# Optimization experiments

Hardware: AMD Instinct MI355X
Metric: run time of the kernel (lower is better)

## Reference

```python
import jax, jax.numpy as jnp
import numpy as np

NODE_IN, EDGE_IN, OUT, EHID, NSTEPS = 74, 13, 64, 128, 6
LN_EPS = 1e-5


def layer_norm(x, gamma, beta):
    mu = jnp.mean(x, axis=-1, keepdims=True)
    var = jnp.mean((x - mu) ** 2, axis=-1, keepdims=True)
    return (x - mu) * jax.lax.rsqrt(var + LN_EPS) * gamma + beta


def setup_inputs() -> dict:
    key = jax.random.key(0)
    ks = jax.random.split(key, 16)
    V, E = 50000, 100000
    inp = {
        "node_feats": jax.random.normal(ks[0], (V, NODE_IN), jnp.float32),
        "edge_feats": jax.random.normal(ks[1], (E, EDGE_IN), jnp.float32),
        "src": jax.random.randint(ks[2], (E,), 0, V, jnp.int32),
        "dst": jax.random.randint(ks[3], (E,), 0, V, jnp.int32),
        # project_node_feats Linear
        "Wp": jax.random.normal(ks[4], (NODE_IN, OUT), jnp.float32) * 0.1,
        "bp": jnp.zeros((OUT,), jnp.float32),
        # edge network MLP: edge_in -> edge_hidden -> out*out
        "We1": jax.random.normal(ks[5], (EDGE_IN, EHID), jnp.float32) * 0.1,
        "be1": jnp.zeros((EHID,), jnp.float32),
        "We2": jax.random.normal(ks[6], (EHID, OUT * OUT), jnp.float32) * 0.02,
        "be2": jnp.zeros((OUT * OUT,), jnp.float32),
        # NNConv bias
        "bconv": jnp.zeros((OUT,), jnp.float32),
        # linearB: 2*out -> out
        "WB": jax.random.normal(ks[7], (2 * OUT, OUT), jnp.float32) * 0.1,
        "bB": jnp.zeros((OUT,), jnp.float32),
        # LayerNorm
        "gamma": jnp.ones((OUT,), jnp.float32),
        "beta": jnp.zeros((OUT,), jnp.float32),
    }
    return inp


def reference(node_feats, edge_feats, src, dst, Wp, bp, We1, be1, We2, be2,
              bconv, WB, bB, gamma, beta):
    V = node_feats.shape[0]
    # project node feats
    h = jax.nn.relu(node_feats @ Wp + bp)  # (V, OUT)
    # per-edge weight matrices (same every step; edge MLP is step-invariant)
    W_e = (jax.nn.relu(edge_feats @ We1 + be1) @ We2 + be2)
    W_e = W_e.reshape(-1, OUT, OUT)  # (E, OUT, OUT)
    for _ in range(NSTEPS):
        msg = jnp.einsum('ei,eio->eo', h[src], W_e)  # gather + per-edge matmul
        agg = jax.ops.segment_sum(msg, dst, num_segments=V) + bconv
        h = jax.nn.relu(agg)
    atom_feats = h
    pair = jnp.concatenate([h[src], h[dst]], axis=1)  # (E, 2*OUT)
    bond_feats = pair @ WB + bB
    atom_out = layer_norm(atom_feats, gamma, beta)
    bond_out = layer_norm(bond_feats, gamma, beta)
    return (atom_out, bond_out)
```

## Files before the change

kernel.cpp:

```cpp
#include <hip/hip_runtime.h>
#include <hip/hip_bf16.h>

typedef __hip_bfloat16 bf16;
typedef __attribute__((ext_vector_type(8))) short bf16x8;
typedef __attribute__((ext_vector_type(4))) float f32x4;

#define NODE_IN 74
#define EDGE_IN 13
#define OUT     64
#define EHID    128
#define NSTEPS  6
#define LN_EPS  1e-5f
#define MB      128
#define NCHUNK  129
#define CHB     16384

__device__ __forceinline__ float ldv(const bf16* p, size_t i) { return __bfloat162float(p[i]); }
__device__ __forceinline__ float ldv(const float* p, size_t i) { return p[i]; }

__device__ __forceinline__ float waveSum(float v) {
    v += __shfl_xor(v, 32);
    v += __shfl_xor(v, 16);
    v += __shfl_xor(v, 8);
    v += __shfl_xor(v, 4);
    v += __shfl_xor(v, 2);
    v += __shfl_xor(v, 1);
    return v;
}

__global__ void detect_kernel(const unsigned int* __restrict__ g, int* __restrict__ flag) {
    if (threadIdx.x == 0 && blockIdx.x == 0)
        *flag = (g[0] == 0x3F803F80u) ? 1 : 0;
}

__global__ void btprep_kernel(const void* We2v, const void* be2v,
                              bf16* __restrict__ BTC, const int* __restrict__ flag) {
    int f = *flag;
    int t = blockIdx.x;
    bf16* out = BTC + (size_t)t * 8192;
    for (int idx = threadIdx.x; idx < 4096; idx += 256) {
        int o = idx >> 6, cw = idx & 63;
        int i = cw ^ ((o & 7) << 3);
        float wv;
        if (t < EHID)
            wv = f ? __bfloat162float(((const bf16*)We2v)[(size_t)t * 4096 + i * 64 + o])
                   : ((const float*)We2v)[(size_t)t * 4096 + i * 64 + o];
        else
            wv = f ? __bfloat162float(((const bf16*)be2v)[i * 64 + o])
                   : ((const float*)be2v)[i * 64 + o];
        bf16 hi = __float2bfloat16(wv);
        out[o * 64 + cw] = hi;
        out[4096 + o * 64 + cw] = __float2bfloat16(wv - __bfloat162float(hi));
    }
}

template <typename T>
__device__ __forceinline__ void proj_body(const T* node, const T* Wp, const T* bp,
                                          float* h, int V) {
    int v = blockIdx.x;
    int o = threadIdx.x;
    __shared__ float nd[NODE_IN];
    for (int i = o; i < NODE_IN; i += 64) nd[i] = ldv(node, (size_t)v * NODE_IN + i);
    __syncthreads();
    float acc = ldv(bp, o);
    for (int i = 0; i < NODE_IN; ++i) acc += nd[i] * ldv(Wp, i * OUT + o);
    h[(size_t)v * OUT + o] = fmaxf(acc, 0.f);
}
__global__ void proj_kernel(const void* node, const void* Wp, const void* bp,
                            float* h, int V, const int* flag) {
    if (*flag) proj_body<bf16>((const bf16*)node, (const bf16*)Wp, (const bf16*)bp, h, V);
    else       proj_body<float>((const float*)node, (const float*)Wp, (const float*)bp, h, V);
}

struct MsgSmem {
    float rs[MB][EHID + 1];
    int dstS[MB];
    __align__(16) char bstage[4][CHB];
};

#define VM4() asm volatile("s_waitcnt vmcnt(4)" ::: "memory")
#define VM2() asm volatile("s_waitcnt vmcnt(2)" ::: "memory")
#define VM0() asm volatile("s_waitcnt vmcnt(0)" ::: "memory")
#define BAR() { __builtin_amdgcn_s_barrier(); asm volatile("" ::: "memory"); }

__device__ __forceinline__ void stage_glds(const char* gbase, char* lbase, int tid) {
#pragma unroll
    for (int c = 0; c < 2; ++c) {
        const void* g = gbase + (size_t)(c * 512 + tid) * 16;
        void* l = lbase + (size_t)(c * 512 + tid) * 16;
        __builtin_amdgcn_global_load_lds(
            (const __attribute__((address_space(1))) void*)g,
            (__attribute__((address_space(3))) void*)l, 16, 0, 0);
    }
}

__device__ __forceinline__ void buildA(float rv, const float (&hv)[8],
                                       bf16x8& phi, bf16x8& plo) {
#pragma unroll
    for (int j = 0; j < 8; ++j) {
        float p = rv * hv[j];
        bf16 hi = __float2bfloat16(p);
        float lof = p - __bfloat162float(hi);
        phi[j] = __builtin_bit_cast(short, hi);
        plo[j] = __builtin_bit_cast(short, __float2bfloat16(lof));
    }
}

#define MFMA_ __builtin_amdgcn_mfma_f32_16x16x32_bf16
#define QUAD(A, B0, B1, B2, B3)        \
    a0 = MFMA_(A, B0, a0, 0, 0, 0);    \
    a1 = MFMA_(A, B1, a1, 0, 0, 0);    \
    a2 = MFMA_(A, B2, a2, 0, 0, 0);    \
    a3 = MFMA_(A, B3, a3, 0, 0, 0);

template <bool SPLITB, typename T>
__device__ __forceinline__ void msg3_body(
    const float* __restrict__ h, const T* __restrict__ ef,
    const T* __restrict__ We1, const T* __restrict__ be1,
    const bf16* __restrict__ BTC, const int* __restrict__ src,
    const int* __restrict__ dst, float* __restrict__ agg, int E, MsgSmem& sm) {
    int e0 = blockIdx.x * MB;
    int tid = threadIdx.x;
    int lane = tid & 63;
    int w = tid >> 6;
    int ne = min(MB, E - e0);
    const char* btc = (const char*)BTC;

    float* We1s = (float*)&sm.bstage[0][0];
    for (int idx = tid; idx < EDGE_IN * EHID; idx += 512)
        We1s[idx] = ldv(We1, idx);
    if (tid < MB) sm.dstS[tid] = (tid < ne) ? dst[e0 + tid] : 0;
    __syncthreads();

    for (int p = 0; p < MB * EHID / 512; ++p) {
        int idx = p * 512 + tid;
        int e = idx >> 7, k = idx & 127;
        float acc = 0.f;
        if (e < ne) {
            acc = ldv(be1, k);
            const T* ep = ef + (size_t)(e0 + e) * EDGE_IN;
#pragma unroll
            for (int i = 0; i < EDGE_IN; ++i)
                acc += ldv(ep, i) * We1s[i * EHID + k];
            acc = fmaxf(acc, 0.f);
        }
        sm.rs[e][k] = acc;
    }
    if (tid < MB) sm.rs[tid][EHID] = (tid < ne) ? 1.f : 0.f;

    int l15 = lane & 15, kq = lane >> 4;
    int r0 = w * 16 + l15;

    float hA[8] = {0}, hB[8] = {0};
    if (r0 < ne) {
        const float* hp = h + (size_t)src[e0 + r0] * OUT + kq * 8;
#pragma unroll
        for (int j = 0; j < 8; ++j) { hA[j] = hp[j]; hB[j] = hp[32 + j]; }
    }
    __syncthreads();

    int offB[8];
#pragma unroll
    for (int s = 0; s < 2; ++s)
#pragma unroll
        for (int cg = 0; cg < 4; ++cg) {
            int row = cg * 16 + l15;
            offB[s * 4 + cg] = (row * 64 + ((s * 32 + kq * 8) ^ ((row & 7) << 3))) * 2;
        }

    f32x4 a0 = {0.f, 0.f, 0.f, 0.f}, a1 = a0, a2 = a0, a3 = a0;

    auto COMPUTE = [&](int t) {
        const char* bp = (const char*)sm.bstage[t & 3];
        float rv = sm.rs[r0][t];
        bf16x8 ph, pl;
        {
            bf16x8 b0 = *(const bf16x8*)(bp + offB[0]);
            bf16x8 b1 = *(const bf16x8*)(bp + offB[1]);
            bf16x8 b2 = *(const bf16x8*)(bp + offB[2]);
            bf16x8 b3 = *(const bf16x8*)(bp + offB[3]);
            buildA(rv, hA, ph, pl);
            QUAD(ph, b0, b1, b2, b3)
            QUAD(pl, b0, b1, b2, b3)
            if (SPLITB) {
                bf16x8 l0 = *(const bf16x8*)(bp + 8192 + offB[0]);
                bf16x8 l1 = *(const bf16x8*)(bp + 8192 + offB[1]);
                bf16x8 l2 = *(const bf16x8*)(bp + 8192 + offB[2]);
                bf16x8 l3 = *(const bf16x8*)(bp + 8192 + offB[3]);
                QUAD(ph, l0, l1, l2, l3)
            }
        }
        {
            bf16x8 b0 = *(const bf16x8*)(bp + offB[4]);
            bf16x8 b1 = *(const bf16x8*)(bp + offB[5]);
            bf16x8 b2 = *(const bf16x8*)(bp + offB[6]);
            bf16x8 b3 = *(const bf16x8*)(bp + offB[7]);
            buildA(rv, hB, ph, pl);
            QUAD(ph, b0, b1, b2, b3)
            QUAD(pl, b0, b1, b2, b3)
            if (SPLITB) {
                bf16x8 l0 = *(const bf16x8*)(bp + 8192 + offB[4]);
                bf16x8 l1 = *(const bf16x8*)(bp + 8192 + offB[5]);
                bf16x8 l2 = *(const bf16x8*)(bp + 8192 + offB[6]);
                bf16x8 l3 = *(const bf16x8*)(bp + 8192 + offB[7]);
                QUAD(ph, l0, l1, l2, l3)
            }
        }
    };

    stage_glds(btc + (size_t)0 * CHB, sm.bstage[0], tid);
    stage_glds(btc + (size_t)1 * CHB, sm.bstage[1], tid);
    stage_glds(btc + (size_t)2 * CHB, sm.bstage[2], tid);
    VM4();
    BAR();

    for (int t = 0; t < NCHUNK - 3; ++t) {
        stage_glds(btc + (size_t)(t + 3) * CHB, sm.bstage[(t + 3) & 3], tid);
        COMPUTE(t);
        VM4();
        BAR();
    }
    COMPUTE(NCHUNK - 3); VM2(); BAR();
    COMPUTE(NCHUNK - 2); VM0(); BAR();
    COMPUTE(NCHUNK - 1);

    int orow = kq * 4;
#pragma unroll
    for (int j = 0; j < 4; ++j) {
        int er = w * 16 + orow + j;
        if (er < ne) {
            float* ap = agg + (size_t)sm.dstS[er] * OUT + l15;
            atomicAdd(ap,      a0[j]);
            atomicAdd(ap + 16, a1[j]);
            atomicAdd(ap + 32, a2[j]);
            atomicAdd(ap + 48, a3[j]);
        }
    }
}

__global__ __launch_bounds__(512) void msg3_kernel(
    const float* h, const void* ef, const void* We1, const void* be1,
    const bf16* BTC, const int* src, const int* dst,
    float* agg, int E, const int* flag) {
    __shared__ MsgSmem sm;
    if (*flag)
        msg3_body<false, bf16>(h, (const bf16*)ef, (const bf16*)We1, (const bf16*)be1,
                               BTC, src, dst, agg, E, sm);
    else
        msg3_body<true, float>(h, (const float*)ef, (const float*)We1, (const float*)be1,
                               BTC, src, dst, agg, E, sm);
}

__global__ void relu_bias_kernel(const float* agg, const void* bconv, float* h, int n,
                                 const int* flag) {
    int f = *flag;
    int idx = blockIdx.x * 256 + threadIdx.x;
    if (idx < n) {
        float b = f ? __bfloat162float(((const bf16*)bconv)[idx & 63])
                    : ((const float*)bconv)[idx & 63];
        h[idx] = fmaxf(agg[idx] + b, 0.f);
    }
}

__global__ void atom_ln_kernel(const float* h, const void* gamma, const void* beta,
                               void* out, int V, const int* flag) {
    int f = *flag;
    int v = blockIdx.x, o = threadIdx.x;
    float x = h[(size_t)v * OUT + o];
    float mu = waveSum(x) * (1.f / 64.f);
    float d = x - mu;
    float var = waveSum(d * d) * (1.f / 64.f);
    float g = f ? __bfloat162float(((const bf16*)gamma)[o]) : ((const float*)gamma)[o];
    float be = f ? __bfloat162float(((const bf16*)beta)[o]) : ((const float*)beta)[o];
    float y = d * rsqrtf(var + LN_EPS) * g + be;
    if (f) ((bf16*)out)[(size_t)v * OUT + o] = __float2bfloat16(y);
    else   ((float*)out)[(size_t)v * OUT + o] = y;
}

__global__ void bond_kernel(const float* h, const int* src, const int* dst,
                            const void* WB, const void* bB, const void* gamma,
                            const void* beta, void* out, int E, int V, const int* flag) {
    int f = *flag;
    int e = blockIdx.x, o = threadIdx.x;
    __shared__ float pair[2 * OUT];
    int s = src[e], d = dst[e];
    pair[o] = h[(size_t)s * OUT + o];
    pair[OUT + o] = h[(size_t)d * OUT + o];
    __syncthreads();
    float acc;
    if (f) {
        acc = __bfloat162float(((const bf16*)bB)[o]);
        for (int j = 0; j < 2 * OUT; ++j)
            acc += pair[j] * __bfloat162float(((const bf16*)WB)[j * OUT + o]);
    } else {
        acc = ((const float*)bB)[o];
        for (int j = 0; j < 2 * OUT; ++j)
            acc += pair[j] * ((const float*)WB)[j * OUT + o];
    }
    float mu = waveSum(acc) * (1.f / 64.f);
    float dd = acc - mu;
    float var = waveSum(dd * dd) * (1.f / 64.f);
    float g = f ? __bfloat162float(((const bf16*)gamma)[o]) : ((const float*)gamma)[o];
    float be = f ? __bfloat162float(((const bf16*)beta)[o]) : ((const float*)beta)[o];
    float y = dd * rsqrtf(var + LN_EPS) * g + be;
    if (f) ((bf16*)out)[(size_t)V * OUT + (size_t)e * OUT + o] = __float2bfloat16(y);
    else   ((float*)out)[(size_t)V * OUT + (size_t)e * OUT + o] = y;
}

extern "C" void kernel_launch(void* const* d_in, const int* in_sizes, int n_in,
                              void* d_out, int out_size, void* d_ws, size_t ws_size,
                              hipStream_t stream) {
    const void* node = d_in[0];
    const void* edgef = d_in[1];
    const int* src = (const int*)d_in[2];
    const int* dst = (const int*)d_in[3];
    const void* Wp = d_in[4];
    const void* bp = d_in[5];
    const void* We1 = d_in[6];
    const void* be1 = d_in[7];
    const void* We2 = d_in[8];
    const void* be2 = d_in[9];
    const void* bconv = d_in[10];
    const void* WB = d_in[11];
    const void* bB = d_in[12];
    const void* gamma = d_in[13];
    const void* beta = d_in[14];

    int V = in_sizes[0] / NODE_IN;
    int E = in_sizes[2];

    char* base = (char*)d_ws;
    int* flag = (int*)base;
    float* h = (float*)(base + 256);
    bf16* BTC = (bf16*)(base + 256 + (size_t)V * OUT * sizeof(float));
    float* agg = (float*)d_out;

    detect_kernel<<<1, 64, 0, stream>>>((const unsigned int*)gamma, flag);
    btprep_kernel<<<NCHUNK, 256, 0, stream>>>(We2, be2, BTC, flag);
    proj_kernel<<<V, 64, 0, stream>>>(node, Wp, bp, h, V, flag);

    int n = V * OUT;
    int nblk = (E + MB - 1) / MB;
    for (int step = 0; step < NSTEPS; ++step) {
        hipMemsetAsync(agg, 0, (size_t)n * sizeof(float), stream);
        msg3_kernel<<<nblk, 512, 0, stream>>>(h, edgef, We1, be1, BTC,
                                              src, dst, agg, E, flag);
        relu_bias_kernel<<<(n + 255) / 256, 256, 0, stream>>>(agg, bconv, h, n, flag);
    }

    atom_ln_kernel<<<V, 64, 0, stream>>>(h, gamma, beta, d_out, V, flag);
    bond_kernel<<<E, 64, 0, stream>>>(h, src, dst, WB, bB, gamma, beta, d_out, E, V, flag);
}
```

Baseline: 2.791 ms.

## Tile message MFMA as 2x2 row/column blocks per wave and fold agg zeroing

Each wave now computes 32 edges by 32 output columns instead of 16 edges by 64 columns. The B fragments loaded from LDS are reused across two edge row-groups, which halves the B LDS reads per MFMA but doubles the A-building (bf16 split) work per wave. Separately, the per-step memset of agg is removed and the relu/bias kernel zeroes agg after reading it. This saves one memset launch and one pass over memory per step, but uses more registers for the doubled h vectors.

```diff
diff --git a/kernel.cpp b/kernel.cpp
--- a/kernel.cpp
+++ b/kernel.cpp
@@ -107,11 +107,6 @@
 }
 
 #define MFMA_ __builtin_amdgcn_mfma_f32_16x16x32_bf16
-#define QUAD(A, B0, B1, B2, B3)        \
-    a0 = MFMA_(A, B0, a0, 0, 0, 0);    \
-    a1 = MFMA_(A, B1, a1, 0, 0, 0);    \
-    a2 = MFMA_(A, B2, a2, 0, 0, 0);    \
-    a3 = MFMA_(A, B3, a3, 0, 0, 0);
 
 template <bool SPLITB, typename T>
 __device__ __forceinline__ void msg3_body(
@@ -149,61 +144,81 @@
     if (tid < MB) sm.rs[tid][EHID] = (tid < ne) ? 1.f : 0.f;
 
     int l15 = lane & 15, kq = lane >> 4;
-    int r0 = w * 16 + l15;
-
-    float hA[8] = {0}, hB[8] = {0};
+    int rp = w >> 1;
+    int cp = w & 1;
+    int r0 = rp * 32 + l15, r1 = r0 + 16;
+
+    float hA0[8] = {0}, hB0[8] = {0}, hA1[8] = {0}, hB1[8] = {0};
     if (r0 < ne) {
         const float* hp = h + (size_t)src[e0 + r0] * OUT + kq * 8;
 #pragma unroll
-        for (int j = 0; j < 8; ++j) { hA[j] = hp[j]; hB[j] = hp[32 + j]; }
+        for (int j = 0; j < 8; ++j) { hA0[j] = hp[j]; hB0[j] = hp[32 + j]; }
+    }
+    if (r1 < ne) {
+        const float* hp = h + (size_t)src[e0 + r1] * OUT + kq * 8;
+#pragma unroll
+        for (int j = 0; j < 8; ++j) { hA1[j] = hp[j]; hB1[j] = hp[32 + j]; }
     }
     __syncthreads();
 
-    int offB[8];
+    int offB[4];
 #pragma unroll
     for (int s = 0; s < 2; ++s)
 #pragma unroll
-        for (int cg = 0; cg < 4; ++cg) {
-            int row = cg * 16 + l15;
-            offB[s * 4 + cg] = (row * 64 + ((s * 32 + kq * 8) ^ ((row & 7) << 3))) * 2;
-        }
-
-    f32x4 a0 = {0.f, 0.f, 0.f, 0.f}, a1 = a0, a2 = a0, a3 = a0;
+        for (int j = 0; j < 2; ++j) {
+            int row = (2 * cp + j) * 16 + l15;
+            offB[s * 2 + j] = (row * 64 + ((s * 32 + kq * 8) ^ ((row & 7) << 3))) * 2;
+        }
+
+    f32x4 a00 = {0.f, 0.f, 0.f, 0.f}, a01 = a00, a10 = a00, a11 = a00;
 
     auto COMPUTE = [&](int t) {
         const char* bp = (const char*)sm.bstage[t & 3];
-        float rv = sm.rs[r0][t];
-        bf16x8 ph, pl;
+        float rv0 = sm.rs[r0][t];
+        float rv1 = sm.rs[r1][t];
+        bf16x8 ph0, pl0, ph1, pl1;
         {
-            bf16x8 b0 = *(const bf16x8*)(bp + offB[0]);
-            bf16x8 b1 = *(const bf16x8*)(bp + offB[1]);
-            bf16x8 b2 = *(const bf16x8*)(bp + offB[2]);
-            bf16x8 b3 = *(const bf16x8*)(bp + offB[3]);
-            buildA(rv, hA, ph, pl);
-            QUAD(ph, b0, b1, b2, b3)
-            QUAD(pl, b0, b1, b2, b3)
+            bf16x8 bh0 = *(const bf16x8*)(bp + offB[0]);
+            bf16x8 bh1 = *(const bf16x8*)(bp + offB[1]);
+            buildA(rv0, hA0, ph0, pl0);
+            buildA(rv1, hA1, ph1, pl1);
+            a00 = MFMA_(ph0, bh0, a00, 0, 0, 0);
+            a01 = MFMA_(ph0, bh1, a01, 0, 0, 0);
+            a00 = MFMA_(pl0, bh0, a00, 0, 0, 0);
+            a01 = MFMA_(pl0, bh1, a01, 0, 0, 0);
+            a10 = MFMA_(ph1, bh0, a10, 0, 0, 0);
+            a11 = MFMA_(ph1, bh1, a11, 0, 0, 0);
+            a10 = MFMA_(pl1, bh0, a10, 0, 0, 0);
+            a11 = MFMA_(pl1, bh1, a11, 0, 0, 0);
             if (SPLITB) {
-                bf16x8 l0 = *(const bf16x8*)(bp + 8192 + offB[0]);
-                bf16x8 l1 = *(const bf16x8*)(bp + 8192 + offB[1]);
-                bf16x8 l2 = *(const bf16x8*)(bp + 8192 + offB[2]);
-                bf16x8 l3 = *(const bf16x8*)(bp + 8192 + offB[3]);
-                QUAD(ph, l0, l1, l2, l3)
+                bf16x8 bl0 = *(const bf16x8*)(bp + 8192 + offB[0]);
+                bf16x8 bl1 = *(const bf16x8*)(bp + 8192 + offB[1]);
+                a00 = MFMA_(ph0, bl0, a00, 0, 0, 0);
+                a01 = MFMA_(ph0, bl1, a01, 0, 0, 0);
+                a10 = MFMA_(ph1, bl0, a10, 0, 0, 0);
+                a11 = MFMA_(ph1, bl1, a11, 0, 0, 0);
             }
         }
         {
-            bf16x8 b0 = *(const bf16x8*)(bp + offB[4]);
-            bf16x8 b1 = *(const bf16x8*)(bp + offB[5]);
-            bf16x8 b2 = *(const bf16x8*)(bp + offB[6]);
-            bf16x8 b3 = *(const bf16x8*)(bp + offB[7]);
-            buildA(rv, hB, ph, pl);
-            QUAD(ph, b0, b1, b2, b3)
-            QUAD(pl, b0, b1, b2, b3)
+            bf16x8 bh0 = *(const bf16x8*)(bp + offB[2]);
+            bf16x8 bh1 = *(const bf16x8*)(bp + offB[3]);
+            buildA(rv0, hB0, ph0, pl0);
+            buildA(rv1, hB1, ph1, pl1);
+            a00 = MFMA_(ph0, bh0, a00, 0, 0, 0);
+            a01 = MFMA_(ph0, bh1, a01, 0, 0, 0);
+            a00 = MFMA_(pl0, bh0, a00, 0, 0, 0);
+            a01 = MFMA_(pl0, bh1, a01, 0, 0, 0);
+            a10 = MFMA_(ph1, bh0, a10, 0, 0, 0);
+            a11 = MFMA_(ph1, bh1, a11, 0, 0, 0);
+            a10 = MFMA_(pl1, bh0, a10, 0, 0, 0);
+            a11 = MFMA_(pl1, bh1, a11, 0, 0, 0);
             if (SPLITB) {
-                bf16x8 l0 = *(const bf16x8*)(bp + 8192 + offB[4]);
-                bf16x8 l1 = *(const bf16x8*)(bp + 8192 + offB[5]);
-                bf16x8 l2 = *(const bf16x8*)(bp + 8192 + offB[6]);
-                bf16x8 l3 = *(const bf16x8*)(bp + 8192 + offB[7]);
-                QUAD(ph, l0, l1, l2, l3)
+                bf16x8 bl0 = *(const bf16x8*)(bp + 8192 + offB[2]);
+                bf16x8 bl1 = *(const bf16x8*)(bp + 8192 + offB[3]);
+                a00 = MFMA_(ph0, bl0, a00, 0, 0, 0);
+                a01 = MFMA_(ph0, bl1, a01, 0, 0, 0);
+                a10 = MFMA_(ph1, bl0, a10, 0, 0, 0);
+                a11 = MFMA_(ph1, bl1, a11, 0, 0, 0);
             }
         }
     };
@@ -225,15 +240,20 @@
     COMPUTE(NCHUNK - 1);
 
     int orow = kq * 4;
+    int colbase = cp * 32 + l15;
 #pragma unroll
     for (int j = 0; j < 4; ++j) {
-        int er = w * 16 + orow + j;
-        if (er < ne) {
-            float* ap = agg + (size_t)sm.dstS[er] * OUT + l15;
-            atomicAdd(ap,      a0[j]);
-            atomicAdd(ap + 16, a1[j]);
-            atomicAdd(ap + 32, a2[j]);
-            atomicAdd(ap + 48, a3[j]);
+        int er0 = rp * 32 + orow + j;
+        if (er0 < ne) {
+            float* ap = agg + (size_t)sm.dstS[er0] * OUT + colbase;
+            atomicAdd(ap,      a00[j]);
+            atomicAdd(ap + 16, a01[j]);
+        }
+        int er1 = rp * 32 + 16 + orow + j;
+        if (er1 < ne) {
+            float* ap = agg + (size_t)sm.dstS[er1] * OUT + colbase;
+            atomicAdd(ap,      a10[j]);
+            atomicAdd(ap + 16, a11[j]);
         }
     }
 }
@@ -251,14 +271,15 @@
                                BTC, src, dst, agg, E, sm);
 }
 
-__global__ void relu_bias_kernel(const float* agg, const void* bconv, float* h, int n,
-                                 const int* flag) {
+__global__ void relu_bias_kernel(const float* agg_r, float* agg_w, const void* bconv,
+                                 float* h, int n, const int* flag) {
     int f = *flag;
     int idx = blockIdx.x * 256 + threadIdx.x;
     if (idx < n) {
         float b = f ? __bfloat162float(((const bf16*)bconv)[idx & 63])
                     : ((const float*)bconv)[idx & 63];
-        h[idx] = fmaxf(agg[idx] + b, 0.f);
+        h[idx] = fmaxf(agg_r[idx] + b, 0.f);
+        agg_w[idx] = 0.f;
     }
 }
 
@@ -341,11 +362,11 @@
 
     int n = V * OUT;
     int nblk = (E + MB - 1) / MB;
+    hipMemsetAsync(agg, 0, (size_t)n * sizeof(float), stream);
     for (int step = 0; step < NSTEPS; ++step) {
-        hipMemsetAsync(agg, 0, (size_t)n * sizeof(float), stream);
         msg3_kernel<<<nblk, 512, 0, stream>>>(h, edgef, We1, be1, BTC,
                                               src, dst, agg, E, flag);
-        relu_bias_kernel<<<(n + 255) / 256, 256, 0, stream>>>(agg, bconv, h, n, flag);
+        relu_bias_kernel<<<(n + 255) / 256, 256, 0, stream>>>(agg, agg, bconv, h, n, flag);
     }
 
     atom_ln_kernel<<<V, 64, 0, stream>>>(h, gamma, beta, d_out, V, flag);
```

Result: slower. 3.166 ms (+13.4%).
